# Kernel optimization log

Measured on AMD Instinct MI355X. Metric: run time of the kernel, lower is better.

## Reference

```python
import jax, jax.numpy as jnp
import numpy as np

T, B, I, H, OUT, NUM_LAYERS, WIN = 256, 256, 128, 512, 128, 3, 32


def _lstm_layer(x, w_ih, w_hh, b):
    """One torch-style LSTM layer. x: [T,B,in] -> hs: [T,B,H].

    Gate order (torch): i, f, g, o. b is b_ih + b_hh.
    """
    Hh = w_hh.shape[1]
    Bb = x.shape[1]
    # Precompute input contribution to gates for all timesteps: [T,B,4H]
    xg = jnp.einsum('tbi,gi->tbg', x, w_ih) + b

    def step(carry, xg_t):
        h, c = carry
        gates = xg_t + h @ w_hh.T            # [B,4H]
        i, f, g, o = jnp.split(gates, 4, axis=-1)
        i = jax.nn.sigmoid(i)
        f = jax.nn.sigmoid(f)
        g = jnp.tanh(g)
        o = jax.nn.sigmoid(o)
        c = f * c + i * g
        h = o * jnp.tanh(c)
        return (h, c), h

    h0 = jnp.zeros((Bb, Hh), x.dtype)
    (_, _), hs = jax.lax.scan(step, (h0, h0), xg)
    return hs


def setup_inputs() -> dict:
    key = jax.random.key(0)
    ks = jax.random.split(key, 12)
    s = 1.0 / np.sqrt(H)  # torch LSTM init scale
    inp = {
        'x': jax.random.normal(ks[0], (T, B, I), jnp.float32),
        'w_ih_0': jax.random.uniform(ks[1], (4 * H, I), jnp.float32, -s, s),
        'w_hh_0': jax.random.uniform(ks[2], (4 * H, H), jnp.float32, -s, s),
        'b_0': jax.random.uniform(ks[3], (4 * H,), jnp.float32, -s, s),
        'w_ih_1': jax.random.uniform(ks[4], (4 * H, H), jnp.float32, -s, s),
        'w_hh_1': jax.random.uniform(ks[5], (4 * H, H), jnp.float32, -s, s),
        'b_1': jax.random.uniform(ks[6], (4 * H,), jnp.float32, -s, s),
        'w_ih_2': jax.random.uniform(ks[7], (4 * H, H), jnp.float32, -s, s),
        'w_hh_2': jax.random.uniform(ks[8], (4 * H, H), jnp.float32, -s, s),
        'b_2': jax.random.uniform(ks[9], (4 * H,), jnp.float32, -s, s),
        'w_out': jax.random.uniform(ks[10], (OUT, H), jnp.float32, -s, s),
        'b_out': jax.random.uniform(ks[11], (OUT,), jnp.float32, -s, s),
        'output_window': WIN,
    }
    return inp


def reference(x, w_ih_0, w_hh_0, b_0, w_ih_1, w_hh_1, b_1,
              w_ih_2, w_hh_2, b_2, w_out, b_out, output_window):
    h = _lstm_layer(x, w_ih_0, w_hh_0, b_0)
    h = _lstm_layer(h, w_ih_1, w_hh_1, b_1)
    h = _lstm_layer(h, w_ih_2, w_hh_2, b_2)
    # Linear on last OutputWindowSize timesteps: [W,B,H] @ [H,OUT]
    y = jnp.einsum('tbh,oh->tbo', h[-output_window:], w_out) + b_out
    return y
```

## Files before the change

### kernel.cpp

```cpp
#include <hip/hip_runtime.h>
#include <hip/hip_bf16.h>
#include <math.h>

#define TT 256
#define BB 256
#define II 128
#define HH 512
#define OO 128
#define WW 32

#define SPIN_CAP 40000

typedef __bf16 bf16x8 __attribute__((ext_vector_type(8)));
typedef float  f32x4  __attribute__((ext_vector_type(4)));

__device__ __forceinline__ float fast_sigm(float x) {
    float e = __builtin_amdgcn_exp2f(-1.442695040889f * x);
    return __builtin_amdgcn_rcpf(1.0f + e);
}
__device__ __forceinline__ float fast_tanh(float x) {
    float e = __builtin_amdgcn_exp2f(2.885390081777f * x);
    return 1.0f - 2.0f * __builtin_amdgcn_rcpf(1.0f + e);
}

__global__ void cast_f32_bf16(const float* __restrict__ in,
                              __bf16* __restrict__ out, int n) {
    int i = blockIdx.x * 256 + threadIdx.x;
    if (i < n) out[i] = (__bf16)in[i];
}

__global__ void pack_w_kernel(const float* __restrict__ wih,
                              const float* __restrict__ whh,
                              __bf16* __restrict__ dst, int KIN) {
    int idx = blockIdx.x * 256 + threadIdx.x;
    int KE8 = (KIN + 512) >> 3;
    int total = 2048 * KE8;
    if (idx >= total) return;
    int row = idx / KE8, k8 = idx - row * KE8;
    int jb = row >> 6, g = (row >> 4) & 3, jj = row & 15;
    int orig = g * 512 + jb * 16 + jj;
    int k = k8 * 8;
    const float* src = (k < KIN) ? (wih + (size_t)orig * KIN + k)
                                 : (whh + (size_t)orig * 512 + (k - KIN));
    __bf16* d = dst + (size_t)row * (KIN + 512) + k;
    #pragma unroll
    for (int i = 0; i < 8; ++i) d[i] = (__bf16)src[i];
}

__device__ __forceinline__ void stage_tile(char* lds, const char* g, int nchunk,
                                           int wv, int l) {
    const int per = nchunk >> 2;
    const char* gp = g + (size_t)l * 16;
    for (int i = 0; i < per; ++i) {
        int c = wv * per + i;
        __builtin_amdgcn_global_load_lds(
            (const __attribute__((address_space(1))) void*)(gp + c * 1024),
            (__attribute__((address_space(3))) void*)(lds + c * 1040),
            16, 0, 0);
    }
}

template <int KX>
__device__ __forceinline__ void run_layer(
    const __bf16* __restrict__ xsrc,
    const __bf16* __restrict__ pw,
    const float*  __restrict__ bias,
    __bf16*       __restrict__ hout,
    int* ctr, int grp, int jb, int tid, int gbase, bool same,
    char* s_x, char* s_h, float (*s_g)[32][18])
{
    const int wv = tid >> 6, l = tid & 63;
    const int KE = KX * 32 + 512;

    bf16x8 w[KX + 16];
    {
        const __bf16* rp = pw + (size_t)(jb * 64 + wv * 16 + (l & 15)) * KE + (l >> 4) * 8;
        #pragma unroll
        for (int kk = 0; kk < KX + 16; ++kk)
            w[kk] = *(const bf16x8*)(rp + kk * 32);
    }

    const int eb = tid >> 3;
    const int ej = (tid & 7) * 2;
    float br[4][2], cc[2];
    #pragma unroll
    for (int g = 0; g < 4; ++g) {
        br[g][0] = bias[g * 512 + jb * 16 + ej];
        br[g][1] = bias[g * 512 + jb * 16 + ej + 1];
    }
    cc[0] = cc[1] = 0.0f;

    const int Cq = (l >> 4) * 16;
    const int row0 = (l & 15), row1 = 16 + (l & 15);
    int xoff0, xoff1;
    if (KX == 4) {
        xoff0 = (row0 >> 2) * 1040 + (row0 & 3) * 256 + Cq;
        xoff1 = (row1 >> 2) * 1040 + (row1 & 3) * 256 + Cq;
    } else {
        xoff0 = row0 * 1040 + Cq;
        xoff1 = row1 * 1040 + Cq;
    }
    const int hoff0 = row0 * 1040 + Cq, hoff1 = row1 * 1040 + Cq;

    const size_t xrow = (size_t)KX * 64;

    stage_tile(s_x, (const char*)xsrc + (size_t)(grp * 32) * xrow, KX * 2, wv, l);
    __syncthreads();

    for (int t = 0; t < TT; ++t) {
        if (t > 0)
            stage_tile(s_h, (const char*)hout + (size_t)((t - 1) * 256 + grp * 32) * 1024,
                       32, wv, l);

        f32x4 acc[2] = {};
        #pragma unroll
        for (int kk = 0; kk < KX; ++kk) {
            bf16x8 a0 = *(const bf16x8*)(s_x + xoff0 + kk * 64);
            bf16x8 a1 = *(const bf16x8*)(s_x + xoff1 + kk * 64);
            acc[0] = __builtin_amdgcn_mfma_f32_16x16x32_bf16(a0, w[kk], acc[0], 0, 0, 0);
            acc[1] = __builtin_amdgcn_mfma_f32_16x16x32_bf16(a1, w[kk], acc[1], 0, 0, 0);
        }
        __syncthreads();
        if (t > 0) {
            #pragma unroll
            for (int kk = 0; kk < 16; ++kk) {
                bf16x8 a0 = *(const bf16x8*)(s_h + hoff0 + kk * 64);
                bf16x8 a1 = *(const bf16x8*)(s_h + hoff1 + kk * 64);
                acc[0] = __builtin_amdgcn_mfma_f32_16x16x32_bf16(a0, w[KX + kk], acc[0], 0, 0, 0);
                acc[1] = __builtin_amdgcn_mfma_f32_16x16x32_bf16(a1, w[KX + kk], acc[1], 0, 0, 0);
            }
        }

        #pragma unroll
        for (int mt = 0; mt < 2; ++mt)
            #pragma unroll
            for (int r = 0; r < 4; ++r)
                s_g[wv][mt * 16 + (l >> 4) * 4 + r][l & 15] = acc[mt][r];
        __syncthreads();

        union { __bf16 h2[2]; unsigned u; } pk;
        #pragma unroll
        for (int q = 0; q < 2; ++q) {
            float xi = s_g[0][eb][ej + q] + br[0][q];
            float xf = s_g[1][eb][ej + q] + br[1][q];
            float xg = s_g[2][eb][ej + q] + br[2][q];
            float xo = s_g[3][eb][ej + q] + br[3][q];
            float iv = fast_sigm(xi), fv = fast_sigm(xf);
            float gv = fast_tanh(xg), ov = fast_sigm(xo);
            cc[q] = (t == 0) ? iv * gv : fmaf(fv, cc[q], iv * gv);
            pk.h2[q] = (__bf16)(ov * fast_tanh(cc[q]));
        }
        *(unsigned*)((char*)hout +
                  (size_t)((t * 256 + grp * 32 + eb) * 512 + jb * 16 + ej) * 2) = pk.u;

        if (!same) __threadfence();
        __syncthreads();
        if (tid == 0)
            __hip_atomic_fetch_add(ctr, 1, __ATOMIC_RELAXED, __HIP_MEMORY_SCOPE_AGENT);
        if (t + 1 < TT)
            stage_tile(s_x, (const char*)xsrc + (size_t)((t + 1) * 256 + grp * 32) * xrow,
                       KX * 2, wv, l);
        if (tid == 0) {
            int tgt = 32 * (gbase + t + 1);
            int spins = 0;
            while (__hip_atomic_load(ctr, __ATOMIC_RELAXED, __HIP_MEMORY_SCOPE_AGENT) < tgt) {
                __builtin_amdgcn_s_sleep(1);
                if (++spins > SPIN_CAP) break;
            }
        }
        __syncthreads();
        if (!same) __threadfence();
    }
}

__global__ __launch_bounds__(256, 1) void lstm_persist(
    const __bf16* __restrict__ xb,
    const __bf16* __restrict__ pw0, const __bf16* __restrict__ pw1,
    const __bf16* __restrict__ pw2,
    const float* __restrict__ b0, const float* __restrict__ b1,
    const float* __restrict__ b2,
    __bf16* __restrict__ h0, __bf16* __restrict__ h1, __bf16* __restrict__ h2,
    int* ctrA, int* hs)
{
    __shared__ __align__(16) char s_x[41600];
    __shared__ __align__(16) char s_h[41600];
    __shared__ float s_g[4][32][18];
    __shared__ int s_grp, s_jb, s_same;

    const int tid = threadIdx.x;

    if (tid == 0) {
        unsigned xcc = 0;
        asm volatile("s_getreg_b32 %0, hwreg(HW_REG_XCC_ID)" : "=s"(xcc));
        xcc &= 7;
        int slot = __hip_atomic_fetch_add(hs + xcc, 1, __ATOMIC_RELAXED,
                                          __HIP_MEMORY_SCOPE_AGENT);
        __hip_atomic_fetch_add(hs + 8, 1, __ATOMIC_RELEASE, __HIP_MEMORY_SCOPE_AGENT);
        int spins = 0;
        while (__hip_atomic_load(hs + 8, __ATOMIC_ACQUIRE, __HIP_MEMORY_SCOPE_AGENT) < 256) {
            __builtin_amdgcn_s_sleep(1);
            if (++spins > SPIN_CAP) break;
        }
        int ok = 1;
        #pragma unroll
        for (int x = 0; x < 8; ++x)
            ok &= (__hip_atomic_load(hs + x, __ATOMIC_RELAXED,
                                     __HIP_MEMORY_SCOPE_AGENT) == 32);
        s_same = ok;
        s_grp = ok ? (int)xcc : (int)(blockIdx.x & 7);
        s_jb  = ok ? slot     : (int)(blockIdx.x >> 3);
    }
    __syncthreads();
    const bool same = (s_same != 0);
    const int  grp  = s_grp, jb = s_jb;

    run_layer<4>(xb, pw0, b0, h0, ctrA + grp * 64, grp, jb, tid, 0, same, s_x, s_h, s_g);
    run_layer<16>(h0, pw1, b1, h1, ctrA + grp * 64, grp, jb, tid, 256, same, s_x, s_h, s_g);
    run_layer<16>(h1, pw2, b2, h2, ctrA + grp * 64, grp, jb, tid, 512, same, s_x, s_h, s_g);
}

__global__ __launch_bounds__(256) void proj_kernel(
    const __bf16* __restrict__ A,
    const __bf16* __restrict__ Wo,
    const float*  __restrict__ bo,
    float*        __restrict__ out)
{
    const int r0   = blockIdx.x * 32;
    const int wave = threadIdx.x >> 6;
    const int lane = threadIdx.x & 63;
    const int n0   = wave * 32;
    const int arow = lane & 15;
    const int koff = (lane >> 4) * 8;

    f32x4 acc[2][2] = {};
    const __bf16* a0p = A  + (size_t)(r0 + arow) * HH + koff;
    const __bf16* a1p = A  + (size_t)(r0 + 16 + arow) * HH + koff;
    const __bf16* w0p = Wo + (size_t)(n0 + arow) * HH + koff;
    const __bf16* w1p = Wo + (size_t)(n0 + 16 + arow) * HH + koff;
    for (int k0 = 0; k0 < HH; k0 += 32) {
        bf16x8 a0 = *(const bf16x8*)(a0p + k0);
        bf16x8 a1 = *(const bf16x8*)(a1p + k0);
        bf16x8 w0 = *(const bf16x8*)(w0p + k0);
        bf16x8 w1 = *(const bf16x8*)(w1p + k0);
        acc[0][0] = __builtin_amdgcn_mfma_f32_16x16x32_bf16(a0, w0, acc[0][0], 0, 0, 0);
        acc[0][1] = __builtin_amdgcn_mfma_f32_16x16x32_bf16(a0, w1, acc[0][1], 0, 0, 0);
        acc[1][0] = __builtin_amdgcn_mfma_f32_16x16x32_bf16(a1, w0, acc[1][0], 0, 0, 0);
        acc[1][1] = __builtin_amdgcn_mfma_f32_16x16x32_bf16(a1, w1, acc[1][1], 0, 0, 0);
    }
    #pragma unroll
    for (int mi = 0; mi < 2; ++mi)
        #pragma unroll
        for (int ni = 0; ni < 2; ++ni)
            #pragma unroll
            for (int r = 0; r < 4; ++r) {
                int row = r0 + mi * 16 + ((lane >> 4) * 4) + r;
                int col = n0 + ni * 16 + (lane & 15);
                out[(size_t)row * OO + col] = acc[mi][ni][r] + bo[col];
            }
}

extern "C" void kernel_launch(void* const* d_in, const int* in_sizes, int n_in,
                              void* d_out, int out_size, void* d_ws, size_t ws_size,
                              hipStream_t stream) {
    const float* x      = (const float*)d_in[0];
    const float* w_ih_0 = (const float*)d_in[1];
    const float* w_hh_0 = (const float*)d_in[2];
    const float* b_0    = (const float*)d_in[3];
    const float* w_ih_1 = (const float*)d_in[4];
    const float* w_hh_1 = (const float*)d_in[5];
    const float* b_1    = (const float*)d_in[6];
    const float* w_ih_2 = (const float*)d_in[7];
    const float* w_hh_2 = (const float*)d_in[8];
    const float* b_2    = (const float*)d_in[9];
    const float* w_out  = (const float*)d_in[10];
    const float* b_out  = (const float*)d_in[11];
    float* out = (float*)d_out;

    char* ws = (char*)d_ws;
    size_t off = 0;
    __bf16* xb    = (__bf16*)(ws + off); off += (size_t)TT * BB * II * 2;
    __bf16* pw0   = (__bf16*)(ws + off); off += (size_t)2048 * 640 * 2;
    __bf16* pw1   = (__bf16*)(ws + off); off += (size_t)2048 * 1024 * 2;
    __bf16* pw2   = (__bf16*)(ws + off); off += (size_t)2048 * 1024 * 2;
    __bf16* woutb = (__bf16*)(ws + off); off += (size_t)OO * HH * 2;
    __bf16* h0    = (__bf16*)(ws + off); off += (size_t)TT * BB * HH * 2;
    __bf16* h1    = (__bf16*)(ws + off); off += (size_t)TT * BB * HH * 2;
    __bf16* h2    = (__bf16*)(ws + off); off += (size_t)TT * BB * HH * 2;
    int*    ctrA  = (int*)(ws + off);    off += (size_t)8 * 64 * 4;
    int*    hs    = (int*)(ws + off);    off += (size_t)64 * 4;
    (void)ws_size; (void)in_sizes; (void)n_in; (void)out_size;

    {
        int n = TT * BB * II;
        cast_f32_bf16<<<(n + 255) / 256, 256, 0, stream>>>(x, xb, n);
        n = OO * HH;
        cast_f32_bf16<<<(n + 255) / 256, 256, 0, stream>>>(w_out, woutb, n);
        int t0 = 2048 * (640 / 8);
        pack_w_kernel<<<(t0 + 255) / 256, 256, 0, stream>>>(w_ih_0, w_hh_0, pw0, II);
        int t1 = 2048 * (1024 / 8);
        pack_w_kernel<<<(t1 + 255) / 256, 256, 0, stream>>>(w_ih_1, w_hh_1, pw1, HH);
        pack_w_kernel<<<(t1 + 255) / 256, 256, 0, stream>>>(w_ih_2, w_hh_2, pw2, HH);
    }
    hipMemsetAsync(ctrA, 0, (size_t)(8 * 64 + 64) * 4, stream);

    lstm_persist<<<256, 256, 0, stream>>>(xb, pw0, pw1, pw2, b_0, b_1, b_2,
                                          h0, h1, h2, ctrA, hs);

    const __bf16* A = h2 + (size_t)(TT - WW) * BB * HH;
    proj_kernel<<<(WW * BB) / 32, 256, 0, stream>>>(A, woutb, b_out, out);
}
```

Before: 2.142 ms.

## Wavefront-pipeline three LSTM layers in one persistent time loop

Measured after the change: 2.475 ms. +15.6%, slower.

```diff
diff --git a/kernel.cpp b/kernel.cpp
--- a/kernel.cpp
+++ b/kernel.cpp
@@ -60,117 +60,43 @@
     }
 }
 
-template <int KX>
-__device__ __forceinline__ void run_layer(
-    const __bf16* __restrict__ xsrc,
-    const __bf16* __restrict__ pw,
-    const float*  __restrict__ bias,
-    __bf16*       __restrict__ hout,
-    int* ctr, int grp, int jb, int tid, int gbase, bool same,
-    char* s_x, char* s_h, float (*s_g)[32][18])
-{
-    const int wv = tid >> 6, l = tid & 63;
-    const int KE = KX * 32 + 512;
-
-    bf16x8 w[KX + 16];
-    {
-        const __bf16* rp = pw + (size_t)(jb * 64 + wv * 16 + (l & 15)) * KE + (l >> 4) * 8;
-        #pragma unroll
-        for (int kk = 0; kk < KX + 16; ++kk)
-            w[kk] = *(const bf16x8*)(rp + kk * 32);
-    }
-
-    const int eb = tid >> 3;
-    const int ej = (tid & 7) * 2;
-    float br[4][2], cc[2];
-    #pragma unroll
-    for (int g = 0; g < 4; ++g) {
-        br[g][0] = bias[g * 512 + jb * 16 + ej];
-        br[g][1] = bias[g * 512 + jb * 16 + ej + 1];
-    }
-    cc[0] = cc[1] = 0.0f;
-
-    const int Cq = (l >> 4) * 16;
-    const int row0 = (l & 15), row1 = 16 + (l & 15);
-    int xoff0, xoff1;
-    if (KX == 4) {
-        xoff0 = (row0 >> 2) * 1040 + (row0 & 3) * 256 + Cq;
-        xoff1 = (row1 >> 2) * 1040 + (row1 & 3) * 256 + Cq;
-    } else {
-        xoff0 = row0 * 1040 + Cq;
-        xoff1 = row1 * 1040 + Cq;
-    }
-    const int hoff0 = row0 * 1040 + Cq, hoff1 = row1 * 1040 + Cq;
-
-    const size_t xrow = (size_t)KX * 64;
-
-    stage_tile(s_x, (const char*)xsrc + (size_t)(grp * 32) * xrow, KX * 2, wv, l);
-    __syncthreads();
-
-    for (int t = 0; t < TT; ++t) {
-        if (t > 0)
-            stage_tile(s_h, (const char*)hout + (size_t)((t - 1) * 256 + grp * 32) * 1024,
-                       32, wv, l);
-
-        f32x4 acc[2] = {};
-        #pragma unroll
-        for (int kk = 0; kk < KX; ++kk) {
-            bf16x8 a0 = *(const bf16x8*)(s_x + xoff0 + kk * 64);
-            bf16x8 a1 = *(const bf16x8*)(s_x + xoff1 + kk * 64);
-            acc[0] = __builtin_amdgcn_mfma_f32_16x16x32_bf16(a0, w[kk], acc[0], 0, 0, 0);
-            acc[1] = __builtin_amdgcn_mfma_f32_16x16x32_bf16(a1, w[kk], acc[1], 0, 0, 0);
-        }
-        __syncthreads();
-        if (t > 0) {
-            #pragma unroll
-            for (int kk = 0; kk < 16; ++kk) {
-                bf16x8 a0 = *(const bf16x8*)(s_h + hoff0 + kk * 64);
-                bf16x8 a1 = *(const bf16x8*)(s_h + hoff1 + kk * 64);
-                acc[0] = __builtin_amdgcn_mfma_f32_16x16x32_bf16(a0, w[KX + kk], acc[0], 0, 0, 0);
-                acc[1] = __builtin_amdgcn_mfma_f32_16x16x32_bf16(a1, w[KX + kk], acc[1], 0, 0, 0);
-            }
-        }
-
-        #pragma unroll
-        for (int mt = 0; mt < 2; ++mt)
-            #pragma unroll
-            for (int r = 0; r < 4; ++r)
-                s_g[wv][mt * 16 + (l >> 4) * 4 + r][l & 15] = acc[mt][r];
-        __syncthreads();
-
-        union { __bf16 h2[2]; unsigned u; } pk;
-        #pragma unroll
-        for (int q = 0; q < 2; ++q) {
-            float xi = s_g[0][eb][ej + q] + br[0][q];
-            float xf = s_g[1][eb][ej + q] + br[1][q];
-            float xg = s_g[2][eb][ej + q] + br[2][q];
-            float xo = s_g[3][eb][ej + q] + br[3][q];
-            float iv = fast_sigm(xi), fv = fast_sigm(xf);
-            float gv = fast_tanh(xg), ov = fast_sigm(xo);
-            cc[q] = (t == 0) ? iv * gv : fmaf(fv, cc[q], iv * gv);
-            pk.h2[q] = (__bf16)(ov * fast_tanh(cc[q]));
-        }
-        *(unsigned*)((char*)hout +
-                  (size_t)((t * 256 + grp * 32 + eb) * 512 + jb * 16 + ej) * 2) = pk.u;
-
-        if (!same) __threadfence();
-        __syncthreads();
-        if (tid == 0)
-            __hip_atomic_fetch_add(ctr, 1, __ATOMIC_RELAXED, __HIP_MEMORY_SCOPE_AGENT);
-        if (t + 1 < TT)
-            stage_tile(s_x, (const char*)xsrc + (size_t)((t + 1) * 256 + grp * 32) * xrow,
-                       KX * 2, wv, l);
-        if (tid == 0) {
-            int tgt = 32 * (gbase + t + 1);
-            int spins = 0;
-            while (__hip_atomic_load(ctr, __ATOMIC_RELAXED, __HIP_MEMORY_SCOPE_AGENT) < tgt) {
-                __builtin_amdgcn_s_sleep(1);
-                if (++spins > SPIN_CAP) break;
-            }
-        }
-        __syncthreads();
-        if (!same) __threadfence();
-    }
+template <int N, int S, int M>
+__device__ __forceinline__ void mm_tile(const char* base, int off0, int off1,
+                                        const bf16x8 (&w)[M], f32x4& a0, f32x4& a1) {
+    #pragma unroll
+    for (int kk = 0; kk < N; ++kk) {
+        bf16x8 x0 = *(const bf16x8*)(base + off0 + kk * 64);
+        bf16x8 x1 = *(const bf16x8*)(base + off1 + kk * 64);
+        a0 = __builtin_amdgcn_mfma_f32_16x16x32_bf16(x0, w[S + kk], a0, 0, 0, 0);
+        a1 = __builtin_amdgcn_mfma_f32_16x16x32_bf16(x1, w[S + kk], a1, 0, 0, 0);
+    }
+}
+
+__device__ __forceinline__ void put_g(float (*sg)[32][18], int wv, int l,
+                                      const f32x4& a0, const f32x4& a1) {
+    #pragma unroll
+    for (int r = 0; r < 4; ++r) {
+        sg[wv][(l >> 4) * 4 + r][l & 15] = a0[r];
+        sg[wv][16 + (l >> 4) * 4 + r][l & 15] = a1[r];
+    }
+}
+
+__device__ __forceinline__ void cell_update(const float (*sg)[32][18],
+                                            const float (&br)[4][2], float (&cc)[2],
+                                            bool first, char* dst, int eb, int ej) {
+    union { __bf16 hv[2]; unsigned u; } pk;
+    #pragma unroll
+    for (int q = 0; q < 2; ++q) {
+        float xi = sg[0][eb][ej + q] + br[0][q];
+        float xf = sg[1][eb][ej + q] + br[1][q];
+        float xg = sg[2][eb][ej + q] + br[2][q];
+        float xo = sg[3][eb][ej + q] + br[3][q];
+        float iv = fast_sigm(xi), fv = fast_sigm(xf);
+        float gv = fast_tanh(xg), ov = fast_sigm(xo);
+        cc[q] = first ? iv * gv : fmaf(fv, cc[q], iv * gv);
+        pk.hv[q] = (__bf16)(ov * fast_tanh(cc[q]));
+    }
+    *(unsigned*)dst = pk.u;
 }
 
 __global__ __launch_bounds__(256, 1) void lstm_persist(
@@ -182,12 +108,15 @@
     __bf16* __restrict__ h0, __bf16* __restrict__ h1, __bf16* __restrict__ h2,
     int* ctrA, int* hs)
 {
-    __shared__ __align__(16) char s_x[41600];
-    __shared__ __align__(16) char s_h[41600];
-    __shared__ float s_g[4][32][18];
+    __shared__ __align__(16) char s_x[8320];
+    __shared__ __align__(16) char s_h0[33280];
+    __shared__ __align__(16) char s_h1[33280];
+    __shared__ __align__(16) char s_h2[33280];
+    __shared__ float s_g0[4][32][18], s_g1[4][32][18], s_g2[4][32][18];
     __shared__ int s_grp, s_jb, s_same;
 
     const int tid = threadIdx.x;
+    const int wv = tid >> 6, l = tid & 63;
 
     if (tid == 0) {
         unsigned xcc = 0;
@@ -213,10 +142,110 @@
     __syncthreads();
     const bool same = (s_same != 0);
     const int  grp  = s_grp, jb = s_jb;
-
-    run_layer<4>(xb, pw0, b0, h0, ctrA + grp * 64, grp, jb, tid, 0, same, s_x, s_h, s_g);
-    run_layer<16>(h0, pw1, b1, h1, ctrA + grp * 64, grp, jb, tid, 256, same, s_x, s_h, s_g);
-    run_layer<16>(h1, pw2, b2, h2, ctrA + grp * 64, grp, jb, tid, 512, same, s_x, s_h, s_g);
+    int* ctr = ctrA + grp * 64;
+
+    bf16x8 w0[20], w1[32], w2[32];
+    {
+        const __bf16* rp = pw0 + (size_t)(jb * 64 + wv * 16 + (l & 15)) * 640 + (l >> 4) * 8;
+        #pragma unroll
+        for (int kk = 0; kk < 20; ++kk) w0[kk] = *(const bf16x8*)(rp + kk * 32);
+    }
+    {
+        const __bf16* rp = pw1 + (size_t)(jb * 64 + wv * 16 + (l & 15)) * 1024 + (l >> 4) * 8;
+        #pragma unroll
+        for (int kk = 0; kk < 32; ++kk) w1[kk] = *(const bf16x8*)(rp + kk * 32);
+    }
+    {
+        const __bf16* rp = pw2 + (size_t)(jb * 64 + wv * 16 + (l & 15)) * 1024 + (l >> 4) * 8;
+        #pragma unroll
+        for (int kk = 0; kk < 32; ++kk) w2[kk] = *(const bf16x8*)(rp + kk * 32);
+    }
+
+    const int eb = tid >> 3;
+    const int ej = (tid & 7) * 2;
+    float br0[4][2], br1[4][2], br2[4][2], cc0[2], cc1[2], cc2[2];
+    #pragma unroll
+    for (int g = 0; g < 4; ++g) {
+        br0[g][0] = b0[g * 512 + jb * 16 + ej]; br0[g][1] = b0[g * 512 + jb * 16 + ej + 1];
+        br1[g][0] = b1[g * 512 + jb * 16 + ej]; br1[g][1] = b1[g * 512 + jb * 16 + ej + 1];
+        br2[g][0] = b2[g * 512 + jb * 16 + ej]; br2[g][1] = b2[g * 512 + jb * 16 + ej + 1];
+    }
+    cc0[0] = cc0[1] = cc1[0] = cc1[1] = cc2[0] = cc2[1] = 0.0f;
+
+    const int Cq = (l >> 4) * 16;
+    const int row0 = (l & 15), row1 = 16 + (l & 15);
+    const int xoff0 = (row0 >> 2) * 1040 + (row0 & 3) * 256 + Cq;
+    const int xoff1 = (row1 >> 2) * 1040 + (row1 & 3) * 256 + Cq;
+    const int hoff0 = row0 * 1040 + Cq;
+    const int hoff1 = row1 * 1040 + Cq;
+
+    const int ebase = jb * 16 + ej;
+
+    stage_tile(s_x, (const char*)xb + (size_t)(grp * 32) * 256, 8, wv, l);
+
+    for (int s = 0; s < TT + 2; ++s) {
+        if (s >= 1 && s <= 256)
+            stage_tile(s_h0, (const char*)h0 + (size_t)((s - 1) * 256 + grp * 32) * 1024,
+                       32, wv, l);
+        if (s >= 2)
+            stage_tile(s_h1, (const char*)h1 + (size_t)((s - 2) * 256 + grp * 32) * 1024,
+                       32, wv, l);
+        if (s >= 3)
+            stage_tile(s_h2, (const char*)h2 + (size_t)((s - 3) * 256 + grp * 32) * 1024,
+                       32, wv, l);
+        __syncthreads();
+
+        if (s < 256) {
+            f32x4 a0 = {}, a1 = {};
+            mm_tile<4, 0>(s_x, xoff0, xoff1, w0, a0, a1);
+            if (s >= 1) mm_tile<16, 4>(s_h0, hoff0, hoff1, w0, a0, a1);
+            put_g(s_g0, wv, l, a0, a1);
+        }
+        if (s >= 1 && s <= 256) {
+            f32x4 a0 = {}, a1 = {};
+            mm_tile<16, 0>(s_h0, hoff0, hoff1, w1, a0, a1);
+            if (s >= 2) mm_tile<16, 16>(s_h1, hoff0, hoff1, w1, a0, a1);
+            put_g(s_g1, wv, l, a0, a1);
+        }
+        if (s >= 2) {
+            f32x4 a0 = {}, a1 = {};
+            mm_tile<16, 0>(s_h1, hoff0, hoff1, w2, a0, a1);
+            if (s >= 3) mm_tile<16, 16>(s_h2, hoff0, hoff1, w2, a0, a1);
+            put_g(s_g2, wv, l, a0, a1);
+        }
+        __syncthreads();
+
+        if (s < 256)
+            cell_update(s_g0, br0, cc0, s == 0,
+                        (char*)h0 + (size_t)((s * 256 + grp * 32 + eb) * 512 + ebase) * 2,
+                        eb, ej);
+        if (s >= 1 && s <= 256)
+            cell_update(s_g1, br1, cc1, s == 1,
+                        (char*)h1 + (size_t)(((s - 1) * 256 + grp * 32 + eb) * 512 + ebase) * 2,
+                        eb, ej);
+        if (s >= 2)
+            cell_update(s_g2, br2, cc2, s == 2,
+                        (char*)h2 + (size_t)(((s - 2) * 256 + grp * 32 + eb) * 512 + ebase) * 2,
+                        eb, ej);
+
+        if (!same) __threadfence();
+        __syncthreads();
+        if (tid == 0)
+            __hip_atomic_fetch_add(ctr, 1, __ATOMIC_RELAXED, __HIP_MEMORY_SCOPE_AGENT);
+        if (s + 1 < 256)
+            stage_tile(s_x, (const char*)xb + (size_t)((s + 1) * 256 + grp * 32) * 256,
+                       8, wv, l);
+        if (tid == 0) {
+            int tgt = 32 * (s + 1);
+            int spins = 0;
+            while (__hip_atomic_load(ctr, __ATOMIC_RELAXED, __HIP_MEMORY_SCOPE_AGENT) < tgt) {
+                __builtin_amdgcn_s_sleep(1);
+                if (++spins > SPIN_CAP) break;
+            }
+        }
+        __syncthreads();
+        if (!same) __threadfence();
+    }
 }
 
 __global__ __launch_bounds__(256) void proj_kernel(
```
